# Optimization experiments

Measured on AMD Instinct MI355X. Metric: run time of the kernel, lower is better.

## Reference

```python
import jax, jax.numpy as jnp
import numpy as np

L = 512      # number of grid points
B = 32768    # batch of independent trajectories


def _rhs(y, w):
    # y: [4, B] -> dy: [4, B]; tiny coupled polynomial vector field
    A, T, N, C = y
    dA = w[0] + w[1] * A + w[2] * A ** 2
    dT = w[3] + w[4] * T + w[5] * T ** 2 + w[6] * A + w[7] * A ** 2 + w[8] * A * T
    dN = w[9] + w[10] * N + w[11] * N ** 2 + w[12] * T + w[13] * T ** 2 + w[14] * T * N
    dC = w[15] + w[16] * C + w[17] * C ** 2 + w[18] * N + w[19] * N ** 2 + w[20] * N * C
    return jnp.stack([dA, dT, dN, dC])


def setup_inputs() -> dict:
    key = jax.random.key(0)
    k1, k2 = jax.random.split(key)
    s_grid = jnp.arange(L, dtype=jnp.float32) * 0.01  # increasing grid, small h
    y0 = jax.random.normal(k1, (4, B), dtype=jnp.float32)
    w = jax.random.normal(k2, (21,), dtype=jnp.float32) * 0.001  # nn.Parameter init
    return {"s_grid": s_grid, "y0": y0, "w": w}


def reference(s_grid, y0, w):
    hs = jnp.diff(s_grid)  # [L-1] step sizes h_i = s[i] - s[i-1]

    def step(y, h):
        y_next = y + h * _rhs(y, w)  # explicit Euler
        return y_next, y_next

    _, ys = jax.lax.scan(step, y0, hs)          # [L-1, 4, B]
    return jnp.concatenate([y0[None], ys], 0)   # [L, 4, B]
```

## Files before the change

### kernel.cpp

```cpp
#include <hip/hip_runtime.h>
#include <hip/hip_bf16.h>


#define ODE_L 512
#define ODE_B 32768

__global__ __launch_bounds__(64) void population_ode_kernel(
    const float* __restrict__ s_grid,
    const float* __restrict__ y0,
    const float* __restrict__ w,
    float* __restrict__ out)
{
    __shared__ float sh_s[ODE_L];

    const int tid = threadIdx.x;
    #pragma unroll
    for (int i = tid; i < ODE_L; i += 64) {
        sh_s[i] = s_grid[i];
    }

    const float w0  = w[0],  w1  = w[1],  w2  = w[2];
    const float w3  = w[3],  w4  = w[4],  w5  = w[5],  w6  = w[6],  w7  = w[7],  w8  = w[8];
    const float w9  = w[9],  w10 = w[10], w11 = w[11], w12 = w[12], w13 = w[13], w14 = w[14];
    const float w15 = w[15], w16 = w[16], w17 = w[17], w18 = w[18], w19 = w[19], w20 = w[20];

    __syncthreads();

    const int b = blockIdx.x * 64 + tid;

    float A = y0[0 * ODE_B + b];
    float T = y0[1 * ODE_B + b];
    float N = y0[2 * ODE_B + b];
    float C = y0[3 * ODE_B + b];

    out[0 * ODE_B + b] = A;
    out[1 * ODE_B + b] = T;
    out[2 * ODE_B + b] = N;
    out[3 * ODE_B + b] = C;

    float s_prev = sh_s[0];

    for (int i = 1; i < ODE_L; ++i) {
        const float s_cur = sh_s[i];
        const float h = s_cur - s_prev;
        s_prev = s_cur;

        const float dA = w0  + w1  * A + w2  * A * A;
        const float dT = w3  + w4  * T + w5  * T * T + w6  * A + w7  * A * A + w8  * A * T;
        const float dN = w9  + w10 * N + w11 * N * N + w12 * T + w13 * T * T + w14 * T * N;
        const float dC = w15 + w16 * C + w17 * C * C + w18 * N + w19 * N * N + w20 * N * C;

        A = A + h * dA;
        T = T + h * dT;
        N = N + h * dN;
        C = C + h * dC;

        const size_t base = (size_t)i * (4 * ODE_B) + (size_t)b;
        out[base + 0 * ODE_B] = A;
        out[base + 1 * ODE_B] = T;
        out[base + 2 * ODE_B] = N;
        out[base + 3 * ODE_B] = C;
    }
}

extern "C" void kernel_launch(void* const* d_in, const int* in_sizes, int n_in,
                              void* d_out, int out_size, void* d_ws, size_t ws_size,
                              hipStream_t stream) {
    (void)in_sizes; (void)n_in; (void)d_ws; (void)ws_size; (void)out_size;

    const float* s_grid = (const float*)d_in[0];
    const float* y0     = (const float*)d_in[1];
    const float* w      = (const float*)d_in[2];
    float* out          = (float*)d_out;

    dim3 grid(ODE_B / 64);
    dim3 block(64);
    population_ode_kernel<<<grid, block, 0, stream>>>(s_grid, y0, w, out);
}
```

Baseline: 272.7 us.

## Split ODE into checkpoint pass and parallel segment replay pass

A first kernel integrates each trajectory without writing the full output and stores state only every 16 steps into workspace. A second kernel launches one block per segment and batch slice, recomputing the 16 steps from the checkpoint and writing the output with far more parallelism. This exposes more concurrent memory traffic than the original 512 single-wave blocks that each serially wrote 512 steps. The cost is extra compute, a second launch, and a checkpoint round trip. Recomputed steps take h as the difference of adjacent s values, the same as before, so results should match. If the workspace is too small it falls back to the original single kernel.

```diff
diff --git a/kernel.cpp b/kernel.cpp
--- a/kernel.cpp
+++ b/kernel.cpp
@@ -4,76 +4,154 @@
 
 #define ODE_L 512
 #define ODE_B 32768
+#define CKPT_STRIDE 16
+#define N_CKPT (ODE_L / CKPT_STRIDE)
+#define CKPT_BYTES ((size_t)N_CKPT * 4 * ODE_B * sizeof(float))
 
-__global__ __launch_bounds__(64) void population_ode_kernel(
+#define LOAD_W() \
+    const float w0  = w[0],  w1  = w[1],  w2  = w[2]; \
+    const float w3  = w[3],  w4  = w[4],  w5  = w[5],  w6  = w[6],  w7  = w[7],  w8  = w[8]; \
+    const float w9  = w[9],  w10 = w[10], w11 = w[11], w12 = w[12], w13 = w[13], w14 = w[14]; \
+    const float w15 = w[15], w16 = w[16], w17 = w[17], w18 = w[18], w19 = w[19], w20 = w[20]
+
+#define EULER_STEP(h) do { \
+    const float dA = w0  + w1  * A + w2  * A * A; \
+    const float dT = w3  + w4  * T + w5  * T * T + w6  * A + w7  * A * A + w8  * A * T; \
+    const float dN = w9  + w10 * N + w11 * N * N + w12 * T + w13 * T * T + w14 * T * N; \
+    const float dC = w15 + w16 * C + w17 * C * C + w18 * N + w19 * N * N + w20 * N * C; \
+    A = A + (h) * dA; \
+    T = T + (h) * dT; \
+    N = N + (h) * dN; \
+    C = C + (h) * dC; \
+} while (0)
+
+__global__ __launch_bounds__(64) void ode_phase1(
     const float* __restrict__ s_grid,
     const float* __restrict__ y0,
     const float* __restrict__ w,
-    float* __restrict__ out)
+    float* __restrict__ ckpt)
 {
-    __shared__ float sh_s[ODE_L];
+    __shared__ float sh_h[ODE_L];
 
     const int tid = threadIdx.x;
-    #pragma unroll
     for (int i = tid; i < ODE_L; i += 64) {
-        sh_s[i] = s_grid[i];
+        const float s0 = s_grid[i];
+        const float s1 = (i < ODE_L - 1) ? s_grid[i + 1] : s0;
+        sh_h[i] = s1 - s0;
     }
 
-    const float w0  = w[0],  w1  = w[1],  w2  = w[2];
-    const float w3  = w[3],  w4  = w[4],  w5  = w[5],  w6  = w[6],  w7  = w[7],  w8  = w[8];
-    const float w9  = w[9],  w10 = w[10], w11 = w[11], w12 = w[12], w13 = w[13], w14 = w[14];
-    const float w15 = w[15], w16 = w[16], w17 = w[17], w18 = w[18], w19 = w[19], w20 = w[20];
-
+    LOAD_W();
     __syncthreads();
 
     const int b = blockIdx.x * 64 + tid;
-
     float A = y0[0 * ODE_B + b];
     float T = y0[1 * ODE_B + b];
     float N = y0[2 * ODE_B + b];
     float C = y0[3 * ODE_B + b];
 
-    out[0 * ODE_B + b] = A;
-    out[1 * ODE_B + b] = T;
-    out[2 * ODE_B + b] = N;
-    out[3 * ODE_B + b] = C;
+    for (int c = 0; c < N_CKPT; ++c) {
+        const size_t cb = (size_t)c * (4 * ODE_B) + (size_t)b;
+        ckpt[cb + 0 * ODE_B] = A;
+        ckpt[cb + 1 * ODE_B] = T;
+        ckpt[cb + 2 * ODE_B] = N;
+        ckpt[cb + 3 * ODE_B] = C;
 
+        const int j0 = c * CKPT_STRIDE;
+        #pragma unroll
+        for (int u = 0; u < CKPT_STRIDE / 4; ++u) {
+            const float4 h4 = *(const float4*)&sh_h[j0 + 4 * u];
+            EULER_STEP(h4.x);
+            EULER_STEP(h4.y);
+            EULER_STEP(h4.z);
+            EULER_STEP(h4.w);
+        }
+    }
+}
+
+__global__ __launch_bounds__(256) void ode_phase2(
+    const float* __restrict__ s_grid,
+    const float* __restrict__ w,
+    const float* __restrict__ ckpt,
+    float* __restrict__ out)
+{
+    __shared__ float sh_s[CKPT_STRIDE];
+
+    const int c  = blockIdx.x;
+    const int i0 = c * CKPT_STRIDE;
+    const int tid = threadIdx.x;
+    if (tid < CKPT_STRIDE) sh_s[tid] = s_grid[i0 + tid];
+
+    LOAD_W();
+    __syncthreads();
+
+    const int b = blockIdx.y * 256 + tid;
+
+    const size_t cb = (size_t)c * (4 * ODE_B) + (size_t)b;
+    float A = ckpt[cb + 0 * ODE_B];
+    float T = ckpt[cb + 1 * ODE_B];
+    float N = ckpt[cb + 2 * ODE_B];
+    float C = ckpt[cb + 3 * ODE_B];
+
+    size_t ob = (size_t)i0 * (4 * ODE_B) + (size_t)b;
+    out[ob + 0 * ODE_B] = A;
+    out[ob + 1 * ODE_B] = T;
+    out[ob + 2 * ODE_B] = N;
+    out[ob + 3 * ODE_B] = C;
+
+    #pragma unroll
+    for (int u = 0; u < CKPT_STRIDE - 1; ++u) {
+        const float h = sh_s[u + 1] - sh_s[u];
+        EULER_STEP(h);
+        const size_t o = ob + (size_t)(u + 1) * (4 * ODE_B);
+        out[o + 0 * ODE_B] = A;
+        out[o + 1 * ODE_B] = T;
+        out[o + 2 * ODE_B] = N;
+        out[o + 3 * ODE_B] = C;
+    }
+}
+
+__global__ __launch_bounds__(64) void ode_single(
+    const float* __restrict__ s_grid, const float* __restrict__ y0,
+    const float* __restrict__ w, float* __restrict__ out)
+{
+    __shared__ float sh_s[ODE_L];
+    const int tid = threadIdx.x;
+    for (int i = tid; i < ODE_L; i += 64) sh_s[i] = s_grid[i];
+    LOAD_W();
+    __syncthreads();
+
+    const int b = blockIdx.x * 64 + tid;
+    float A = y0[0 * ODE_B + b], T = y0[1 * ODE_B + b];
+    float N = y0[2 * ODE_B + b], C = y0[3 * ODE_B + b];
+    out[0 * ODE_B + b] = A; out[1 * ODE_B + b] = T;
+    out[2 * ODE_B + b] = N; out[3 * ODE_B + b] = C;
     float s_prev = sh_s[0];
-
     for (int i = 1; i < ODE_L; ++i) {
         const float s_cur = sh_s[i];
         const float h = s_cur - s_prev;
         s_prev = s_cur;
-
-        const float dA = w0  + w1  * A + w2  * A * A;
-        const float dT = w3  + w4  * T + w5  * T * T + w6  * A + w7  * A * A + w8  * A * T;
-        const float dN = w9  + w10 * N + w11 * N * N + w12 * T + w13 * T * T + w14 * T * N;
-        const float dC = w15 + w16 * C + w17 * C * C + w18 * N + w19 * N * N + w20 * N * C;
-
-        A = A + h * dA;
-        T = T + h * dT;
-        N = N + h * dN;
-        C = C + h * dC;
-
+        EULER_STEP(h);
         const size_t base = (size_t)i * (4 * ODE_B) + (size_t)b;
-        out[base + 0 * ODE_B] = A;
-        out[base + 1 * ODE_B] = T;
-        out[base + 2 * ODE_B] = N;
-        out[base + 3 * ODE_B] = C;
+        out[base + 0 * ODE_B] = A; out[base + 1 * ODE_B] = T;
+        out[base + 2 * ODE_B] = N; out[base + 3 * ODE_B] = C;
     }
 }
 
 extern "C" void kernel_launch(void* const* d_in, const int* in_sizes, int n_in,
                               void* d_out, int out_size, void* d_ws, size_t ws_size,
                               hipStream_t stream) {
-    (void)in_sizes; (void)n_in; (void)d_ws; (void)ws_size; (void)out_size;
+    (void)in_sizes; (void)n_in; (void)out_size;
 
     const float* s_grid = (const float*)d_in[0];
     const float* y0     = (const float*)d_in[1];
     const float* w      = (const float*)d_in[2];
     float* out          = (float*)d_out;
 
-    dim3 grid(ODE_B / 64);
-    dim3 block(64);
-    population_ode_kernel<<<grid, block, 0, stream>>>(s_grid, y0, w, out);
+    if (ws_size >= CKPT_BYTES) {
+        float* ckpt = (float*)d_ws;
+        ode_phase1<<<dim3(ODE_B / 64), dim3(64), 0, stream>>>(s_grid, y0, w, ckpt);
+        ode_phase2<<<dim3(N_CKPT, ODE_B / 256), dim3(256), 0, stream>>>(s_grid, w, ckpt, out);
+    } else {
+        ode_single<<<dim3(ODE_B / 64), dim3(64), 0, stream>>>(s_grid, y0, w, out);
+    }
 }
```

New measurement: 312.3 us. +14.5%, slower.
